# Kernel optimization log

Hardware: AMD Instinct MI355X
Metric: run time of the kernel (lower is better)

The kernel has to match this reference:

```python
import jax, jax.numpy as jnp
import numpy as np

B, T, D, H, L = 4, 128, 768, 770, 40  # batch, token_num, bert dim, head hidden, n_labels


def setup_inputs() -> dict:
    key = jax.random.key(0)
    ks = jax.random.split(key, 7)
    hidden = jax.random.normal(ks[0], (B, T + 1, D), dtype=jnp.float32)
    pred_spans = jnp.sort(jax.random.randint(ks[1], (B, 2), 0, T), axis=1)
    span_avail = jax.random.randint(ks[2], (T, T), 0, 2).astype(jnp.int32)
    # torch nn.Linear: weight init N(0, 0.02), bias init N(0, 1) (normal_(bias, 0) -> mean=0, std=1)
    W1 = (jax.random.normal(ks[3], (2 * D + 1, H)) * 0.02).astype(jnp.float32)
    b1 = jax.random.normal(ks[4], (H,), dtype=jnp.float32)
    W2 = (jax.random.normal(ks[5], (H, L)) * 0.02).astype(jnp.float32)
    b2 = jax.random.normal(ks[6], (L,), dtype=jnp.float32)
    return {"hidden": hidden, "W1": W1, "b1": b1, "W2": W2, "b2": b2,
            "pred_spans": pred_spans, "span_avail": span_avail, "token_num": T}


def reference(hidden, W1, b1, W2, b2, pred_spans, span_avail, token_num):
    # vecs[i] = hidden[:, i+1, :]  (skip [CLS])
    vecs = hidden[:, 1:token_num + 1, :]                      # [B, T, D]
    Bv, Tv, Dv = vecs.shape
    starts = pred_spans[:, 0][:, None, None]                  # [B,1,1]
    ends = pred_spans[:, 1][:, None, None]
    ii = jnp.arange(Tv)[:, None]                              # [T,1]
    jj = jnp.arange(Tv)[None, :]                              # [1,T]
    # indication: 2 if (i,j) == pred span; 1 if strictly inside span with i<=j; else 0
    is_full = (ii == starts) & (jj == ends)                   # [B,T,T]
    inside = (starts <= ii) & (ii <= jj) & (jj <= ends) & (~is_full)
    ind = (2 * is_full + inside).astype(hidden.dtype)         # [B,T,T]
    fi = jnp.broadcast_to(vecs[:, :, None, :], (Bv, Tv, Tv, Dv))
    fj = jnp.broadcast_to(vecs[:, None, :, :], (Bv, Tv, Tv, Dv))
    feat = jnp.concatenate([fi, fj, ind[..., None]], axis=-1)  # [B,T,T,2D+1]
    h = jax.nn.relu(feat @ W1 + b1)                            # [B,T,T,H]
    out = h @ W2 + b2                                          # [B,T,T,L]
    # unavailable spans contribute a zeros row (original appends `zeros`)
    mask = (span_avail >= 1)[None, :, :, None]
    out = jnp.where(mask, out, jnp.zeros((), out.dtype))
    out = out.reshape(Bv, Tv * Tv, -1)                         # span index c = i*T + j
    return jax.nn.log_softmax(out, axis=1)
```

## Files before the change

kernel.cpp:

```cpp
#include <hip/hip_runtime.h>
#include <math.h>

#define BB 4
#define TT 128
#define DD 768
#define HD 770
#define HP 800
#define LL 40
#define TP1 129

typedef __attribute__((ext_vector_type(8))) short s16x8;
typedef __attribute__((ext_vector_type(4))) float f32x4;

#define P_OFF   0
#define Q_OFF   409600
#define W2F_OFF 819200
#define ACC_OFF 838400

__device__ __forceinline__ unsigned pkbf(float a, float b) {
    unsigned ua = __float_as_uint(a);
    unsigned ub = __float_as_uint(b);
    return ((ua + 0x8000u) >> 16) | ((ub + 0x8000u) & 0xffff0000u);
}
__device__ __forceinline__ unsigned rne1(float v) {
    unsigned x = __float_as_uint(v);
    return (x + 0x7fffu + ((x >> 16) & 1u)) >> 16;
}

__global__ __launch_bounds__(256) void kA(const float* __restrict__ hidden,
                                          const float* __restrict__ W1,
                                          const float* __restrict__ W2,
                                          const float* __restrict__ b1,
                                          float* __restrict__ P,
                                          float* __restrict__ Q,
                                          unsigned* __restrict__ W2f,
                                          float* __restrict__ accum) {
    __shared__ uint4 Bl[3072];
    const int bx  = blockIdx.x;
    const int tid = threadIdx.x;

    if (bx < 392) {
        const int nt = bx / 8;
        const int mg = bx - nt * 8;
        const int lane = tid & 63;
        const int col  = lane & 15;
        const int quad = lane >> 4;

        for (int u = tid; u < 3072; u += 256) {
            int half = u / 1536;
            int rem  = u - half * 1536;
            int ks = rem >> 6;
            int ln = rem & 63;
            int kbase = ks * 32 + ((ln >> 4) << 3);
            int h = nt * 16 + (ln & 15);
            int row0 = half * DD + kbase;
            unsigned pk[4];
            #pragma unroll
            for (int sp = 0; sp < 4; ++sp) {
                unsigned w[2];
                #pragma unroll
                for (int e = 0; e < 2; ++e) {
                    float v = (h < HD) ? W1[(size_t)(row0 + 2 * sp + e) * HD + h] : 0.0f;
                    w[e] = rne1(v);
                }
                pk[sp] = w[0] | (w[1] << 16);
            }
            Bl[u] = make_uint4(pk[0], pk[1], pk[2], pk[3]);
        }
        __syncthreads();

        const int mband = mg * 4 + (tid >> 6);
        const int b  = mband >> 3;
        const int tt = mband & 7;

        const float* __restrict__ Arow =
            hidden + (size_t)(b * TP1 + 1 + tt * 16 + col) * DD + (quad << 3);

        f32x4 a0 = (f32x4){0.f, 0.f, 0.f, 0.f};
        f32x4 a1 = (f32x4){0.f, 0.f, 0.f, 0.f};

        #pragma unroll 4
        for (int ks = 0; ks < 24; ++ks) {
            float4 x0 = *(const float4*)(Arow + ks * 32);
            float4 x1 = *(const float4*)(Arow + ks * 32 + 4);
            union { unsigned u[4]; s16x8 v; } af;
            af.u[0] = pkbf(x0.x, x0.y); af.u[1] = pkbf(x0.z, x0.w);
            af.u[2] = pkbf(x1.x, x1.y); af.u[3] = pkbf(x1.z, x1.w);
            union { uint4 q; s16x8 v; } bf0, bf1;
            bf0.q = Bl[ks * 64 + lane];
            bf1.q = Bl[1536 + ks * 64 + lane];
            a0 = __builtin_amdgcn_mfma_f32_16x16x32_bf16(af.v, bf0.v, a0, 0, 0, 0);
            a1 = __builtin_amdgcn_mfma_f32_16x16x32_bf16(af.v, bf1.v, a1, 0, 0, 0);
        }

        const int h = nt * 16 + col;
        if (h < HD) {
            const float bv = b1[h];
            #pragma unroll
            for (int r = 0; r < 4; ++r) {
                int t = tt * 16 + quad * 4 + r;
                size_t row = (size_t)(b * TT + t) * HP;
                P[row + h] = a0[r] + bv;
                Q[row + h] = a1[r];
            }
        }
    } else if (bx < 411) {
        int u = (bx - 392) * 256 + tid;
        if (u >= 4800) return;
        int nt = u / 1600;
        int rem = u - nt * 1600;
        int ks = rem >> 6;
        int ln = rem & 63;
        int kbase = ks * 32 + ((ln >> 4) << 3);
        int l = nt * 16 + (ln & 15);
        unsigned pk[4];
        #pragma unroll
        for (int sp = 0; sp < 4; ++sp) {
            unsigned w[2];
            #pragma unroll
            for (int e = 0; e < 2; ++e) {
                int k = kbase + 2 * sp + e;
                float v = (k < HD && l < LL) ? W2[k * LL + l] : 0.0f;
                w[e] = rne1(v);
            }
            pk[sp] = w[0] | (w[1] << 16);
        }
        ((uint4*)W2f)[u] = make_uint4(pk[0], pk[1], pk[2], pk[3]);
    } else if (bx == 411) {
        if (tid < 160) accum[tid] = 0.0f;
    } else {
        int u = (bx - 412) * 256 + tid;
        int row = u / 30;
        int h = HD + (u - row * 30);
        Q[(size_t)row * HP + h] = 0.0f;
    }
}

__global__ __launch_bounds__(256) void kB(const float* __restrict__ P,
                                          const float* __restrict__ Q,
                                          const float* __restrict__ W1,
                                          const unsigned* __restrict__ W2f,
                                          const float* __restrict__ b2,
                                          const int* __restrict__ spans,
                                          const int* __restrict__ avail,
                                          float* __restrict__ out,
                                          float* __restrict__ accum) {
    __shared__ unsigned Sb[2][128 * 20];
    __shared__ float var[3 * HP];
    __shared__ int avi[TT];
    __shared__ float sred[192];

    const int i = blockIdx.x;
    const int b = blockIdx.y;
    const int tid = threadIdx.x;
    const int wave = tid >> 6;
    const int lane = tid & 63;

    const int start = spans[b * 2];
    const int end   = spans[b * 2 + 1];

    const int jS = tid >> 1;
    const int hh = (tid & 1) << 4;
    int indS;
    {
        bool isfull = (i == start) && (jS == end);
        bool inside = (start <= i) && (i <= jS) && (jS <= end) && !isfull;
        indS = isfull ? 2 : (inside ? 1 : 0);
    }

    {
        const float* Pi  = P + (size_t)(b * TT + i) * HP;
        const float* w1L = W1 + (size_t)2 * DD * HD;
        for (int h = tid; h < HP; h += 256) {
            float pv = (h < HD) ? Pi[h] : 0.0f;
            float wv = (h < HD) ? w1L[h] : 0.0f;
            var[h]        = pv;
            var[HP + h]   = pv + wv;
            var[2*HP + h] = pv + wv + wv;
        }
        if (tid < TT) avi[tid] = avail[i * TT + tid];
    }
    __syncthreads();

    const float* Qj = Q + (size_t)(b * TT + jS) * HP;
    const float* vb = var + indS * HP;

    auto form = [&](int c, int p) {
        const int h0 = c * 32 + hh;
        const float4* qp = (const float4*)(Qj + h0);
        float4 q0 = qp[0], q1 = qp[1], q2 = qp[2], q3 = qp[3];
        const float4* vp = (const float4*)(vb + h0);
        float4 v0 = vp[0], v1 = vp[1], v2 = vp[2], v3 = vp[3];
        float s0 = fmaxf(v0.x + q0.x, 0.f), s1 = fmaxf(v0.y + q0.y, 0.f);
        float s2 = fmaxf(v0.z + q0.z, 0.f), s3 = fmaxf(v0.w + q0.w, 0.f);
        float s4 = fmaxf(v1.x + q1.x, 0.f), s5 = fmaxf(v1.y + q1.y, 0.f);
        float s6 = fmaxf(v1.z + q1.z, 0.f), s7 = fmaxf(v1.w + q1.w, 0.f);
        float s8 = fmaxf(v2.x + q2.x, 0.f), s9 = fmaxf(v2.y + q2.y, 0.f);
        float sa = fmaxf(v2.z + q2.z, 0.f), sb_ = fmaxf(v2.w + q2.w, 0.f);
        float sc = fmaxf(v3.x + q3.x, 0.f), sd = fmaxf(v3.y + q3.y, 0.f);
        float se = fmaxf(v3.z + q3.z, 0.f), sf = fmaxf(v3.w + q3.w, 0.f);
        uint4* dst = (uint4*)(&Sb[p][jS * 20 + (hh >> 1)]);
        dst[0] = make_uint4(pkbf(s0,s1), pkbf(s2,s3), pkbf(s4,s5), pkbf(s6,s7));
        dst[1] = make_uint4(pkbf(s8,s9), pkbf(sa,sb_), pkbf(sc,sd), pkbf(se,sf));
    };

    f32x4 acc[2][3];
    #pragma unroll
    for (int mt = 0; mt < 2; ++mt)
        #pragma unroll
        for (int nt = 0; nt < 3; ++nt)
            acc[mt][nt] = (f32x4){0.f, 0.f, 0.f, 0.f};

    form(0, 0);
    __syncthreads();

    const int arow0 = (wave * 32 + (lane & 15)) * 20 + ((lane >> 4) << 2);
    for (int c = 0; c < 25; ++c) {
        const int p = c & 1;
        s16x8 bf0 = *(const s16x8*)((const unsigned*)W2f + (( 0 + c) * 64 + lane) * 4);
        s16x8 bf1 = *(const s16x8*)((const unsigned*)W2f + ((25 + c) * 64 + lane) * 4);
        s16x8 bf2 = *(const s16x8*)((const unsigned*)W2f + ((50 + c) * 64 + lane) * 4);
        s16x8 af0 = *(const s16x8*)(&Sb[p][arow0]);
        s16x8 af1 = *(const s16x8*)(&Sb[p][arow0 + 16 * 20]);
        if (c + 1 < 25) form(c + 1, p ^ 1);
        acc[0][0] = __builtin_amdgcn_mfma_f32_16x16x32_bf16(af0, bf0, acc[0][0], 0, 0, 0);
        acc[0][1] = __builtin_amdgcn_mfma_f32_16x16x32_bf16(af0, bf1, acc[0][1], 0, 0, 0);
        acc[0][2] = __builtin_amdgcn_mfma_f32_16x16x32_bf16(af0, bf2, acc[0][2], 0, 0, 0);
        acc[1][0] = __builtin_amdgcn_mfma_f32_16x16x32_bf16(af1, bf0, acc[1][0], 0, 0, 0);
        acc[1][1] = __builtin_amdgcn_mfma_f32_16x16x32_bf16(af1, bf1, acc[1][1], 0, 0, 0);
        acc[1][2] = __builtin_amdgcn_mfma_f32_16x16x32_bf16(af1, bf2, acc[1][2], 0, 0, 0);
        __syncthreads();
    }

    float bias[3];
    #pragma unroll
    for (int nt = 0; nt < 3; ++nt) {
        int l = nt * 16 + (lane & 15);
        bias[nt] = (l < LL) ? b2[l] : 0.0f;
    }
    const int jr0 = wave * 32 + ((lane >> 4) << 2);
    float sE[3] = {0.f, 0.f, 0.f};
    #pragma unroll
    for (int mt = 0; mt < 2; ++mt) {
        #pragma unroll
        for (int r = 0; r < 4; ++r) {
            int j = jr0 + mt * 16 + r;
            bool msk = avi[j] >= 1;
            size_t rowoff = ((size_t)(b * (TT * TT) + i * TT + j)) * LL;
            #pragma unroll
            for (int nt = 0; nt < 3; ++nt) {
                int l = nt * 16 + (lane & 15);
                if (l < LL) {
                    float val = msk ? (acc[mt][nt][r] + bias[nt]) : 0.0f;
                    out[rowoff + l] = val;
                    sE[nt] += __expf(val);
                }
            }
        }
    }
    #pragma unroll
    for (int nt = 0; nt < 3; ++nt) {
        float v = sE[nt];
        v += __shfl_xor(v, 16);
        v += __shfl_xor(v, 32);
        if (lane < 16) sred[wave * 48 + nt * 16 + lane] = v;
    }
    __syncthreads();
    if (tid < 48) {
        float t4 = sred[tid] + sred[48 + tid] + sred[96 + tid] + sred[144 + tid];
        if (tid < LL) atomicAdd(&accum[b * LL + tid], t4);
    }
}

__global__ __launch_bounds__(256) void kD(float* __restrict__ out,
                                          const float* __restrict__ accum) {
    const int idx = blockIdx.x * 256 + threadIdx.x;
    const int e = idx * 4;
    const int b = e / (TT * TT * LL);
    const int l = e % LL;
    float4 v = ((float4*)out)[idx];
    const float* ac = accum + b * LL + l;
    v.x -= __logf(ac[0]); v.y -= __logf(ac[1]);
    v.z -= __logf(ac[2]); v.w -= __logf(ac[3]);
    ((float4*)out)[idx] = v;
}

extern "C" void kernel_launch(void* const* d_in, const int* in_sizes, int n_in,
                              void* d_out, int out_size, void* d_ws, size_t ws_size,
                              hipStream_t stream) {
    const float* hidden = (const float*)d_in[0];
    const float* W1     = (const float*)d_in[1];
    const float* b1     = (const float*)d_in[2];
    const float* W2     = (const float*)d_in[3];
    const float* b2     = (const float*)d_in[4];
    const int*   spans  = (const int*)d_in[5];
    const int*   avail  = (const int*)d_in[6];
    float* out = (float*)d_out;
    float* ws  = (float*)d_ws;

    float*    P     = ws + P_OFF;
    float*    Q     = ws + Q_OFF;
    unsigned* W2f   = (unsigned*)(ws + W2F_OFF);
    float*    accum = ws + ACC_OFF;

    kA <<<dim3(472),    dim3(256), 0, stream>>>(hidden, W1, W2, b1, P, Q, W2f, accum);
    kB <<<dim3(TT, BB), dim3(256), 0, stream>>>(P, Q, W1, W2f, b2, spans, avail, out, accum);
    kD <<<dim3(2560),   dim3(256), 0, stream>>>(out, accum);
}
```

Baseline: 125.4 us.

## Prefetch Q chunks into registers one step ahead and lighten loop barriers

```diff
diff --git a/kernel.cpp b/kernel.cpp
--- a/kernel.cpp
+++ b/kernel.cpp
@@ -25,6 +25,9 @@
 __device__ __forceinline__ unsigned rne1(float v) {
     unsigned x = __float_as_uint(v);
     return (x + 0x7fffu + ((x >> 16) & 1u)) >> 16;
+}
+__device__ __forceinline__ void ldsbar() {
+    asm volatile("s_waitcnt lgkmcnt(0)\n\ts_barrier" ::: "memory");
 }
 
 __global__ __launch_bounds__(256) void kA(const float* __restrict__ hidden,
@@ -180,29 +183,39 @@
         }
         if (tid < TT) avi[tid] = avail[i * TT + tid];
     }
-    __syncthreads();
 
     const float* Qj = Q + (size_t)(b * TT + jS) * HP;
     const float* vb = var + indS * HP;
 
-    auto form = [&](int c, int p) {
+    auto pack = [&](int c, int p, float4 qa, float4 qb) {
         const int h0 = c * 32 + hh;
-        const float4* qp = (const float4*)(Qj + h0);
-        float4 q0 = qp[0], q1 = qp[1], q2 = qp[2], q3 = qp[3];
+        const float4* vp = (const float4*)(vb + h0);
+        float4 v0 = vp[0], v1 = vp[1];
+        float s0 = fmaxf(v0.x + qa.x, 0.f), s1 = fmaxf(v0.y + qa.y, 0.f);
+        float s2 = fmaxf(v0.z + qa.z, 0.f), s3 = fmaxf(v0.w + qa.w, 0.f);
+        float s4 = fmaxf(v1.x + qb.x, 0.f), s5 = fmaxf(v1.y + qb.y, 0.f);
+        float s6 = fmaxf(v1.z + qb.z, 0.f), s7 = fmaxf(v1.w + qb.w, 0.f);
+        uint4* dst = (uint4*)(&Sb[p][jS * 20 + (hh >> 1)]);
+        dst[0] = make_uint4(pkbf(s0,s1), pkbf(s2,s3), pkbf(s4,s5), pkbf(s6,s7));
+    };
+
+    auto pack2 = [&](int c, int p, float4 qa, float4 qb, float4 qc, float4 qd) {
+        const int h0 = c * 32 + hh;
         const float4* vp = (const float4*)(vb + h0);
         float4 v0 = vp[0], v1 = vp[1], v2 = vp[2], v3 = vp[3];
-        float s0 = fmaxf(v0.x + q0.x, 0.f), s1 = fmaxf(v0.y + q0.y, 0.f);
-        float s2 = fmaxf(v0.z + q0.z, 0.f), s3 = fmaxf(v0.w + q0.w, 0.f);
-        float s4 = fmaxf(v1.x + q1.x, 0.f), s5 = fmaxf(v1.y + q1.y, 0.f);
-        float s6 = fmaxf(v1.z + q1.z, 0.f), s7 = fmaxf(v1.w + q1.w, 0.f);
-        float s8 = fmaxf(v2.x + q2.x, 0.f), s9 = fmaxf(v2.y + q2.y, 0.f);
-        float sa = fmaxf(v2.z + q2.z, 0.f), sb_ = fmaxf(v2.w + q2.w, 0.f);
-        float sc = fmaxf(v3.x + q3.x, 0.f), sd = fmaxf(v3.y + q3.y, 0.f);
-        float se = fmaxf(v3.z + q3.z, 0.f), sf = fmaxf(v3.w + q3.w, 0.f);
+        float s0 = fmaxf(v0.x + qa.x, 0.f), s1 = fmaxf(v0.y + qa.y, 0.f);
+        float s2 = fmaxf(v0.z + qa.z, 0.f), s3 = fmaxf(v0.w + qa.w, 0.f);
+        float s4 = fmaxf(v1.x + qb.x, 0.f), s5 = fmaxf(v1.y + qb.y, 0.f);
+        float s6 = fmaxf(v1.z + qb.z, 0.f), s7 = fmaxf(v1.w + qb.w, 0.f);
+        float s8 = fmaxf(v2.x + qc.x, 0.f), s9 = fmaxf(v2.y + qc.y, 0.f);
+        float sa = fmaxf(v2.z + qc.z, 0.f), sb_ = fmaxf(v2.w + qc.w, 0.f);
+        float sc = fmaxf(v3.x + qd.x, 0.f), sd = fmaxf(v3.y + qd.y, 0.f);
+        float se = fmaxf(v3.z + qd.z, 0.f), sf = fmaxf(v3.w + qd.w, 0.f);
         uint4* dst = (uint4*)(&Sb[p][jS * 20 + (hh >> 1)]);
         dst[0] = make_uint4(pkbf(s0,s1), pkbf(s2,s3), pkbf(s4,s5), pkbf(s6,s7));
         dst[1] = make_uint4(pkbf(s8,s9), pkbf(sa,sb_), pkbf(sc,sd), pkbf(se,sf));
     };
+    (void)pack;
 
     f32x4 acc[2][3];
     #pragma unroll
@@ -211,10 +224,18 @@
         for (int nt = 0; nt < 3; ++nt)
             acc[mt][nt] = (f32x4){0.f, 0.f, 0.f, 0.f};
 
-    form(0, 0);
+    float4 ca, cb, cc, cd;
+    {
+        const float4* qp = (const float4*)(Qj + hh);
+        float4 a0 = qp[0], a1 = qp[1], a2 = qp[2], a3 = qp[3];
+        pack2(0, 0, a0, a1, a2, a3);
+        const float4* qn = (const float4*)(Qj + 32 + hh);
+        ca = qn[0]; cb = qn[1]; cc = qn[2]; cd = qn[3];
+    }
     __syncthreads();
 
     const int arow0 = (wave * 32 + (lane & 15)) * 20 + ((lane >> 4) << 2);
+    #pragma unroll
     for (int c = 0; c < 25; ++c) {
         const int p = c & 1;
         s16x8 bf0 = *(const s16x8*)((const unsigned*)W2f + (( 0 + c) * 64 + lane) * 4);
@@ -222,14 +243,21 @@
         s16x8 bf2 = *(const s16x8*)((const unsigned*)W2f + ((50 + c) * 64 + lane) * 4);
         s16x8 af0 = *(const s16x8*)(&Sb[p][arow0]);
         s16x8 af1 = *(const s16x8*)(&Sb[p][arow0 + 16 * 20]);
-        if (c + 1 < 25) form(c + 1, p ^ 1);
+        if (c + 1 < 25) {
+            float4 fa = ca, fb = cb, fc = cc, fd = cd;
+            if (c + 2 < 25) {
+                const float4* qn = (const float4*)(Qj + (c + 2) * 32 + hh);
+                ca = qn[0]; cb = qn[1]; cc = qn[2]; cd = qn[3];
+            }
+            pack2(c + 1, p ^ 1, fa, fb, fc, fd);
+        }
         acc[0][0] = __builtin_amdgcn_mfma_f32_16x16x32_bf16(af0, bf0, acc[0][0], 0, 0, 0);
         acc[0][1] = __builtin_amdgcn_mfma_f32_16x16x32_bf16(af0, bf1, acc[0][1], 0, 0, 0);
         acc[0][2] = __builtin_amdgcn_mfma_f32_16x16x32_bf16(af0, bf2, acc[0][2], 0, 0, 0);
         acc[1][0] = __builtin_amdgcn_mfma_f32_16x16x32_bf16(af1, bf0, acc[1][0], 0, 0, 0);
         acc[1][1] = __builtin_amdgcn_mfma_f32_16x16x32_bf16(af1, bf1, acc[1][1], 0, 0, 0);
         acc[1][2] = __builtin_amdgcn_mfma_f32_16x16x32_bf16(af1, bf2, acc[1][2], 0, 0, 0);
-        __syncthreads();
+        ldsbar();
     }
 
     float bias[3];
```

After: 121.7 us. 2.9% less time.

## Split kB rows across two blocks with wave-local LDS staging and Q prefetch

Applied to the files above, without the earlier changes.

```diff
diff --git a/kernel.cpp b/kernel.cpp
--- a/kernel.cpp
+++ b/kernel.cpp
@@ -25,6 +25,9 @@
 __device__ __forceinline__ unsigned rne1(float v) {
     unsigned x = __float_as_uint(v);
     return (x + 0x7fffu + ((x >> 16) & 1u)) >> 16;
+}
+__device__ __forceinline__ void ldswait() {
+    asm volatile("s_waitcnt lgkmcnt(0)" ::: "memory");
 }
 
 __global__ __launch_bounds__(256) void kA(const float* __restrict__ hidden,
@@ -145,28 +148,22 @@
                                           const int* __restrict__ avail,
                                           float* __restrict__ out,
                                           float* __restrict__ accum) {
-    __shared__ unsigned Sb[2][128 * 20];
+    __shared__ unsigned Sb[2][64 * 20];
     __shared__ float var[3 * HP];
-    __shared__ int avi[TT];
+    __shared__ int avi[64];
     __shared__ float sred[192];
 
-    const int i = blockIdx.x;
-    const int b = blockIdx.y;
+    const int jh = blockIdx.x;
+    const int i  = blockIdx.y;
+    const int b  = blockIdx.z;
     const int tid = threadIdx.x;
     const int wave = tid >> 6;
     const int lane = tid & 63;
+    const int col  = lane & 15;
+    const int quad = lane >> 4;
 
     const int start = spans[b * 2];
     const int end   = spans[b * 2 + 1];
-
-    const int jS = tid >> 1;
-    const int hh = (tid & 1) << 4;
-    int indS;
-    {
-        bool isfull = (i == start) && (jS == end);
-        bool inside = (start <= i) && (i <= jS) && (jS <= end) && !isfull;
-        indS = isfull ? 2 : (inside ? 1 : 0);
-    }
 
     {
         const float* Pi  = P + (size_t)(b * TT + i) * HP;
@@ -178,83 +175,89 @@
             var[HP + h]   = pv + wv;
             var[2*HP + h] = pv + wv + wv;
         }
-        if (tid < TT) avi[tid] = avail[i * TT + tid];
+        if (tid < 64) avi[tid] = avail[i * TT + jh * 64 + tid];
     }
     __syncthreads();
 
-    const float* Qj = Q + (size_t)(b * TT + jS) * HP;
+    const int jloc = tid >> 2;
+    const int jS   = jh * 64 + jloc;
+    const int hh   = (tid & 3) << 3;
+    int indS;
+    {
+        bool f = (i == start) && (jS == end);
+        indS = f ? 2 : (((start <= i) && (i <= jS) && (jS <= end)) ? 1 : 0);
+    }
+    const float* __restrict__ Qj = Q + (size_t)(b * TT + jS) * HP;
     const float* vb = var + indS * HP;
-
-    auto form = [&](int c, int p) {
+    const int sdst = jloc * 20 + ((tid & 3) << 2);
+
+    auto pack8 = [&](int c, int p, float4 qa, float4 qb) {
         const int h0 = c * 32 + hh;
-        const float4* qp = (const float4*)(Qj + h0);
-        float4 q0 = qp[0], q1 = qp[1], q2 = qp[2], q3 = qp[3];
-        const float4* vp = (const float4*)(vb + h0);
-        float4 v0 = vp[0], v1 = vp[1], v2 = vp[2], v3 = vp[3];
-        float s0 = fmaxf(v0.x + q0.x, 0.f), s1 = fmaxf(v0.y + q0.y, 0.f);
-        float s2 = fmaxf(v0.z + q0.z, 0.f), s3 = fmaxf(v0.w + q0.w, 0.f);
-        float s4 = fmaxf(v1.x + q1.x, 0.f), s5 = fmaxf(v1.y + q1.y, 0.f);
-        float s6 = fmaxf(v1.z + q1.z, 0.f), s7 = fmaxf(v1.w + q1.w, 0.f);
-        float s8 = fmaxf(v2.x + q2.x, 0.f), s9 = fmaxf(v2.y + q2.y, 0.f);
-        float sa = fmaxf(v2.z + q2.z, 0.f), sb_ = fmaxf(v2.w + q2.w, 0.f);
-        float sc = fmaxf(v3.x + q3.x, 0.f), sd = fmaxf(v3.y + q3.y, 0.f);
-        float se = fmaxf(v3.z + q3.z, 0.f), sf = fmaxf(v3.w + q3.w, 0.f);
-        uint4* dst = (uint4*)(&Sb[p][jS * 20 + (hh >> 1)]);
-        dst[0] = make_uint4(pkbf(s0,s1), pkbf(s2,s3), pkbf(s4,s5), pkbf(s6,s7));
-        dst[1] = make_uint4(pkbf(s8,s9), pkbf(sa,sb_), pkbf(sc,sd), pkbf(se,sf));
+        float4 v0 = *(const float4*)(vb + h0);
+        float4 v1 = *(const float4*)(vb + h0 + 4);
+        float s0 = fmaxf(v0.x + qa.x, 0.f), s1 = fmaxf(v0.y + qa.y, 0.f);
+        float s2 = fmaxf(v0.z + qa.z, 0.f), s3 = fmaxf(v0.w + qa.w, 0.f);
+        float s4 = fmaxf(v1.x + qb.x, 0.f), s5 = fmaxf(v1.y + qb.y, 0.f);
+        float s6 = fmaxf(v1.z + qb.z, 0.f), s7 = fmaxf(v1.w + qb.w, 0.f);
+        *(uint4*)(&Sb[p][sdst]) =
+            make_uint4(pkbf(s0,s1), pkbf(s2,s3), pkbf(s4,s5), pkbf(s6,s7));
     };
 
-    f32x4 acc[2][3];
-    #pragma unroll
-    for (int mt = 0; mt < 2; ++mt)
-        #pragma unroll
-        for (int nt = 0; nt < 3; ++nt)
-            acc[mt][nt] = (f32x4){0.f, 0.f, 0.f, 0.f};
-
-    form(0, 0);
-    __syncthreads();
-
-    const int arow0 = (wave * 32 + (lane & 15)) * 20 + ((lane >> 4) << 2);
+    f32x4 acc[3];
+    #pragma unroll
+    for (int nt = 0; nt < 3; ++nt) acc[nt] = (f32x4){0.f, 0.f, 0.f, 0.f};
+
+    float4 ca, cb;
+    {
+        const float4* qp = (const float4*)(Qj + hh);
+        pack8(0, 0, qp[0], qp[1]);
+        const float4* qn = (const float4*)(Qj + 32 + hh);
+        ca = qn[0]; cb = qn[1];
+    }
+    ldswait();
+
+    const int arow0 = (wave * 16 + col) * 20 + (quad << 2);
+    #pragma unroll
     for (int c = 0; c < 25; ++c) {
         const int p = c & 1;
         s16x8 bf0 = *(const s16x8*)((const unsigned*)W2f + (( 0 + c) * 64 + lane) * 4);
         s16x8 bf1 = *(const s16x8*)((const unsigned*)W2f + ((25 + c) * 64 + lane) * 4);
         s16x8 bf2 = *(const s16x8*)((const unsigned*)W2f + ((50 + c) * 64 + lane) * 4);
-        s16x8 af0 = *(const s16x8*)(&Sb[p][arow0]);
-        s16x8 af1 = *(const s16x8*)(&Sb[p][arow0 + 16 * 20]);
-        if (c + 1 < 25) form(c + 1, p ^ 1);
-        acc[0][0] = __builtin_amdgcn_mfma_f32_16x16x32_bf16(af0, bf0, acc[0][0], 0, 0, 0);
-        acc[0][1] = __builtin_amdgcn_mfma_f32_16x16x32_bf16(af0, bf1, acc[0][1], 0, 0, 0);
-        acc[0][2] = __builtin_amdgcn_mfma_f32_16x16x32_bf16(af0, bf2, acc[0][2], 0, 0, 0);
-        acc[1][0] = __builtin_amdgcn_mfma_f32_16x16x32_bf16(af1, bf0, acc[1][0], 0, 0, 0);
-        acc[1][1] = __builtin_amdgcn_mfma_f32_16x16x32_bf16(af1, bf1, acc[1][1], 0, 0, 0);
-        acc[1][2] = __builtin_amdgcn_mfma_f32_16x16x32_bf16(af1, bf2, acc[1][2], 0, 0, 0);
-        __syncthreads();
+        s16x8 af  = *(const s16x8*)(&Sb[p][arow0]);
+        if (c + 1 < 25) {
+            float4 fa = ca, fb = cb;
+            if (c + 2 < 25) {
+                const float4* qn = (const float4*)(Qj + (c + 2) * 32 + hh);
+                ca = qn[0]; cb = qn[1];
+            }
+            pack8(c + 1, p ^ 1, fa, fb);
+        }
+        acc[0] = __builtin_amdgcn_mfma_f32_16x16x32_bf16(af, bf0, acc[0], 0, 0, 0);
+        acc[1] = __builtin_amdgcn_mfma_f32_16x16x32_bf16(af, bf1, acc[1], 0, 0, 0);
+        acc[2] = __builtin_amdgcn_mfma_f32_16x16x32_bf16(af, bf2, acc[2], 0, 0, 0);
+        ldswait();
     }
 
     float bias[3];
     #pragma unroll
     for (int nt = 0; nt < 3; ++nt) {
-        int l = nt * 16 + (lane & 15);
+        int l = nt * 16 + col;
         bias[nt] = (l < LL) ? b2[l] : 0.0f;
     }
-    const int jr0 = wave * 32 + ((lane >> 4) << 2);
     float sE[3] = {0.f, 0.f, 0.f};
     #pragma unroll
-    for (int mt = 0; mt < 2; ++mt) {
+    for (int r = 0; r < 4; ++r) {
+        int aj = wave * 16 + quad * 4 + r;
+        int j  = jh * 64 + aj;
+        bool msk = avi[aj] >= 1;
+        size_t rowoff = ((size_t)(b * (TT * TT) + i * TT + j)) * LL;
         #pragma unroll
-        for (int r = 0; r < 4; ++r) {
-            int j = jr0 + mt * 16 + r;
-            bool msk = avi[j] >= 1;
-            size_t rowoff = ((size_t)(b * (TT * TT) + i * TT + j)) * LL;
-            #pragma unroll
-            for (int nt = 0; nt < 3; ++nt) {
-                int l = nt * 16 + (lane & 15);
-                if (l < LL) {
-                    float val = msk ? (acc[mt][nt][r] + bias[nt]) : 0.0f;
-                    out[rowoff + l] = val;
-                    sE[nt] += __expf(val);
-                }
+        for (int nt = 0; nt < 3; ++nt) {
+            int l = nt * 16 + col;
+            if (l < LL) {
+                float val = msk ? (acc[nt][r] + bias[nt]) : 0.0f;
+                out[rowoff + l] = val;
+                sE[nt] += __expf(val);
             }
         }
     }
@@ -303,7 +306,7 @@
     unsigned* W2f   = (unsigned*)(ws + W2F_OFF);
     float*    accum = ws + ACC_OFF;
 
-    kA <<<dim3(472),    dim3(256), 0, stream>>>(hidden, W1, W2, b1, P, Q, W2f, accum);
-    kB <<<dim3(TT, BB), dim3(256), 0, stream>>>(P, Q, W1, W2f, b2, spans, avail, out, accum);
-    kD <<<dim3(2560),   dim3(256), 0, stream>>>(out, accum);
-}
+    kA <<<dim3(472),        dim3(256), 0, stream>>>(hidden, W1, W2, b1, P, Q, W2f, accum);
+    kB <<<dim3(2, TT, BB),  dim3(256), 0, stream>>>(P, Q, W1, W2f, b2, spans, avail, out, accum);
+    kD <<<dim3(2560),       dim3(256), 0, stream>>>(out, accum);
+}
```

Result: no change. 125.8 us (+0.4%).
